# Performance work log

Hardware: AMD Instinct MI355X
Metric: run time of the kernel (lower is better)

The kernel has to match this reference:

```python
import jax, jax.numpy as jnp
import numpy as np

TOP_K = 50
MIN_KEEP = 5
TOP_P = 0.8
TEMPERATURE = 1.0
PENALTY = 1.1
LN_EPS = 1e-5

B, HIST, H, V = 32, 2048, 2048, 128000


def setup_inputs() -> dict:
    key = jax.random.key(0)
    k1, k2, k3, k4, k5 = jax.random.split(key, 5)
    hidden_states = jax.random.normal(k1, (B, H), dtype=jnp.float32)
    input_ids = jax.random.randint(k2, (B, HIST), 0, V, dtype=jnp.int64)
    ln_gamma = 1.0 + 0.02 * jax.random.normal(k3, (H,), dtype=jnp.float32)
    ln_beta = 0.02 * jax.random.normal(k4, (H,), dtype=jnp.float32)
    W = 0.02 * jax.random.normal(k5, (V, H), dtype=jnp.float32)  # lm_head weight [vocab, hidden]
    return {"input_ids": input_ids, "hidden_states": hidden_states,
            "ln_gamma": ln_gamma, "ln_beta": ln_beta, "W": W}


def reference(input_ids, hidden_states, ln_gamma, ln_beta, W):
    # ln_f: LayerNorm over hidden dim
    mu = jnp.mean(hidden_states, axis=-1, keepdims=True)
    var = jnp.mean(jnp.square(hidden_states - mu), axis=-1, keepdims=True)
    h = (hidden_states - mu) * jax.lax.rsqrt(var + LN_EPS) * ln_gamma + ln_beta
    # lm_head: [B,H] @ [H,V] -> [B,V]
    m_logits = jnp.einsum('bh,vh->bv', h, W)
    # repetition penalty: gather logits at history ids, penalize, scatter back
    g = jnp.take_along_axis(m_logits, input_ids, axis=1)          # [B, HIST]
    pen = jnp.where(g < 0, g * PENALTY, g / PENALTY)
    m_logits = jax.vmap(lambda row, idx, val: row.at[idx].set(val))(m_logits, input_ids, pen)
    # top-k, temperature, nucleus (top-p) masking
    vals, token = jax.lax.top_k(m_logits.astype(jnp.float32), TOP_K)  # [B, TOP_K]
    vals = vals / TEMPERATURE
    cum = jnp.cumsum(jax.nn.softmax(vals, axis=1), axis=1)
    keep = jnp.arange(TOP_K) < MIN_KEEP                            # keep_matrix row
    mask = (cum < TOP_P) | keep
    filtered = jnp.where(mask, vals, jnp.float32(-1000.0))
    probs = jax.nn.softmax(filtered, axis=1)
    return (probs, token)
```

## Files before the change

kernel.cpp:

```cpp
#include <hip/hip_runtime.h>
#include <math.h>

#define B_    32
#define H_    2048
#define V_    128000
#define HIST_ 2048
#define TOPK  50

__global__ __launch_bounds__(256) void ln_kernel(const float* __restrict__ x,
        const float* __restrict__ gamma, const float* __restrict__ beta,
        float* __restrict__ h) {
    int b = blockIdx.x, t = threadIdx.x;
    const float* xr = x + b * H_;
    __shared__ float red[4];
    __shared__ float sval;
    float s = 0.f;
    for (int k = t; k < H_; k += 256) s += xr[k];
    #pragma unroll
    for (int o = 32; o; o >>= 1) s += __shfl_down(s, o);
    if ((t & 63) == 0) red[t >> 6] = s;
    __syncthreads();
    if (t == 0) sval = (red[0] + red[1] + red[2] + red[3]) * (1.f / H_);
    __syncthreads();
    float mu = sval;
    float v = 0.f;
    for (int k = t; k < H_; k += 256) { float d = xr[k] - mu; v += d * d; }
    #pragma unroll
    for (int o = 32; o; o >>= 1) v += __shfl_down(v, o);
    if ((t & 63) == 0) red[t >> 6] = v;
    __syncthreads();
    if (t == 0) sval = 1.f / sqrtf((red[0] + red[1] + red[2] + red[3]) * (1.f / H_) + 1e-5f);
    __syncthreads();
    float rstd = sval;
    for (int k = t; k < H_; k += 256)
        h[b * H_ + k] = (xr[k] - mu) * rstd * gamma[k] + beta[k];
}

#define VT  256
#define KC  32
#define NCH (H_ / KC)

__global__ __launch_bounds__(256, 2) void gemm_kernel(const float* __restrict__ Wm,
        const float* __restrict__ hs, float* __restrict__ logits) {
    __shared__ float ldsW[VT * KC];
    __shared__ float ldsH[KC * B_];
    const int t  = threadIdx.x;
    const int v0 = blockIdx.x * VT;

    float acc[B_];
    #pragma unroll
    for (int i = 0; i < B_; i++) acc[i] = 0.f;

    float4 wreg[8];
    float4 hreg;
    const int hb = t >> 3, hk = (t & 7) * 4;

    #pragma unroll
    for (int i = 0; i < 8; i++) {
        int g = i * 256 + t, r = g >> 3, p = g & 7;
        wreg[i] = *(const float4*)(Wm + (size_t)(v0 + r) * H_ + p * 4);
    }
    hreg = *(const float4*)(hs + hb * H_ + hk);

    for (int c = 0; c < NCH; c++) {
        #pragma unroll
        for (int i = 0; i < 8; i++) {
            int g = i * 256 + t, r = g >> 3, p = g & 7;
            *(float4*)&ldsW[r * KC + ((p ^ (r & 7)) << 2)] = wreg[i];
        }
        ldsH[(hk + 0) * B_ + hb] = hreg.x;
        ldsH[(hk + 1) * B_ + hb] = hreg.y;
        ldsH[(hk + 2) * B_ + hb] = hreg.z;
        ldsH[(hk + 3) * B_ + hb] = hreg.w;
        __syncthreads();

        if (c + 1 < NCH) {
            int kn = (c + 1) * KC;
            #pragma unroll
            for (int i = 0; i < 8; i++) {
                int g = i * 256 + t, r = g >> 3, p = g & 7;
                wreg[i] = *(const float4*)(Wm + (size_t)(v0 + r) * H_ + kn + p * 4);
            }
            hreg = *(const float4*)(hs + hb * H_ + kn + hk);
        }

        for (int q = 0; q < KC / 4; q++) {
            float4 w4 = *(const float4*)&ldsW[t * KC + ((q ^ (t & 7)) << 2)];
            float wk[4] = {w4.x, w4.y, w4.z, w4.w};
            #pragma unroll
            for (int j = 0; j < 4; j++) {
                const float4* hp = (const float4*)&ldsH[(q * 4 + j) * B_];
                #pragma unroll
                for (int g2 = 0; g2 < 8; g2++) {
                    float4 hv = hp[g2];
                    acc[g2 * 4 + 0] += wk[j] * hv.x;
                    acc[g2 * 4 + 1] += wk[j] * hv.y;
                    acc[g2 * 4 + 2] += wk[j] * hv.z;
                    acc[g2 * 4 + 3] += wk[j] * hv.w;
                }
            }
        }
        __syncthreads();
    }

    const int v = v0 + t;
    #pragma unroll
    for (int b = 0; b < B_; b++)
        logits[(size_t)b * V_ + v] = acc[b];
}

__global__ __launch_bounds__(256) void pen_gather(const int* __restrict__ ids,
        const float* __restrict__ logits, float* __restrict__ pen) {
    int i = blockIdx.x * 256 + threadIdx.x;
    int b = i >> 11;
    int id = ids[i];
    float g = logits[(size_t)b * V_ + id];
    pen[i] = (g < 0.f) ? g * 1.1f : g / 1.1f;
}
__global__ __launch_bounds__(256) void pen_scatter(const int* __restrict__ ids,
        float* __restrict__ logits, const float* __restrict__ pen) {
    int i = blockIdx.x * 256 + threadIdx.x;
    int b = i >> 11;
    logits[(size_t)b * V_ + ids[i]] = pen[i];
}

__device__ __forceinline__ unsigned f2k(float f) {
    unsigned u = __float_as_uint(f);
    return (u >> 31) ? ~u : (u | 0x80000000u);
}
__device__ __forceinline__ float k2f(unsigned k) {
    return __uint_as_float((k >> 31) ? (k ^ 0x80000000u) : ~k);
}

__global__ __launch_bounds__(256) void topk_kernel(const float* __restrict__ logits,
        float* __restrict__ out) {
    int b = blockIdx.x, t = threadIdx.x;
    const float* row = logits + (size_t)b * V_;
    __shared__ int hist[256];
    __shared__ int sB1, sC1, sB2, sNa, sNe;
    __shared__ unsigned gtK[64];  __shared__ int gtI[64];
    __shared__ unsigned eqK[256]; __shared__ int eqI[256];
    __shared__ float outv[TOPK];  __shared__ int outi[TOPK];

    hist[t] = 0;
    __syncthreads();
    for (int v = t; v < V_; v += 256) atomicAdd(&hist[f2k(row[v]) >> 24], 1);
    __syncthreads();
    if (t == 0) {
        int c = 0, i = 255;
        for (; i >= 0; i--) { if (c + hist[i] >= TOPK) break; c += hist[i]; }
        sB1 = i; sC1 = c;
    }
    __syncthreads();
    unsigned b1 = (unsigned)sB1; int c1 = sC1;

    hist[t] = 0;
    __syncthreads();
    for (int v = t; v < V_; v += 256) {
        unsigned k = f2k(row[v]);
        if ((k >> 24) == b1) atomicAdd(&hist[(k >> 16) & 255], 1);
    }
    __syncthreads();
    if (t == 0) {
        int c = c1, i = 255;
        for (; i >= 0; i--) { if (c + hist[i] >= TOPK) break; c += hist[i]; }
        sB2 = i; sNa = 0; sNe = 0;
    }
    __syncthreads();
    unsigned pref = (b1 << 8) | (unsigned)sB2;

    for (int v = t; v < V_; v += 256) {
        unsigned k = f2k(row[v]);
        unsigned t16 = k >> 16;
        if (t16 > pref)       { int p = atomicAdd(&sNa, 1); if (p < 64)  { gtK[p] = k; gtI[p] = v; } }
        else if (t16 == pref) { int p = atomicAdd(&sNe, 1); if (p < 256) { eqK[p] = k; eqI[p] = v; } }
    }
    __syncthreads();

    if (t == 0) {
        int na = sNa; if (na > TOPK) na = TOPK;
        for (int i = 1; i < na; i++) {
            unsigned k = gtK[i]; int id = gtI[i]; int j = i - 1;
            for (; j >= 0 && (gtK[j] < k || (gtK[j] == k && gtI[j] > id)); j--) {
                gtK[j + 1] = gtK[j]; gtI[j + 1] = gtI[j];
            }
            gtK[j + 1] = k; gtI[j + 1] = id;
        }
        for (int i = 0; i < na; i++) { outv[i] = k2f(gtK[i]); outi[i] = gtI[i]; }
        int ne = sNe; if (ne > 256) ne = 256;
        for (int s = na; s < TOPK; s++) {
            int best = -1; unsigned bk = 0; int bi = 0x7fffffff;
            for (int i = 0; i < ne; i++) {
                if (eqI[i] < 0) continue;
                if (best < 0 || eqK[i] > bk || (eqK[i] == bk && eqI[i] < bi)) {
                    best = i; bk = eqK[i]; bi = eqI[i];
                }
            }
            outv[s] = k2f(bk); outi[s] = bi; eqI[best] = -1;
        }
    }
    __syncthreads();

    if (t < 64) {
        int i = t;
        float m  = outv[0];
        float vi = (i < TOPK) ? outv[i] : 0.f;
        float e  = (i < TOPK) ? expf(vi - m) : 0.f;
        float tot = e;
        #pragma unroll
        for (int o = 1; o < 64; o <<= 1) tot += __shfl_xor(tot, o);
        float p = e / tot;
        float pre = p;
        #pragma unroll
        for (int o = 1; o < 64; o <<= 1) { float u = __shfl_up(pre, o); if (t >= o) pre += u; }
        bool keep = (pre < 0.8f) || (i < 5);
        float f  = keep ? vi : -1000.f;
        float e2 = (i < TOPK) ? expf(f - m) : 0.f;
        float tot2 = e2;
        #pragma unroll
        for (int o = 1; o < 64; o <<= 1) tot2 += __shfl_xor(tot2, o);
        if (i < TOPK) {
            out[b * TOPK + i] = e2 / tot2;
            out[B_ * TOPK + b * TOPK + i] = (float)outi[i];
        }
    }
}

extern "C" void kernel_launch(void* const* d_in, const int* in_sizes, int n_in,
                              void* d_out, int out_size, void* d_ws, size_t ws_size,
                              hipStream_t stream) {
    const int*   ids    = (const int*)d_in[0];
    const float* hidden = (const float*)d_in[1];
    const float* gamma  = (const float*)d_in[2];
    const float* beta   = (const float*)d_in[3];
    const float* Wm     = (const float*)d_in[4];
    float* out = (float*)d_out;

    char* ws = (char*)d_ws;
    float* h      = (float*)ws;
    float* logits = (float*)(ws + 262144);
    float* pen    = (float*)(ws + 262144 + 16384000);

    ln_kernel  <<<B_,        256, 0, stream>>>(hidden, gamma, beta, h);
    gemm_kernel<<<V_ / VT,   256, 0, stream>>>(Wm, h, logits);
    pen_gather <<<(B_*HIST_)/256, 256, 0, stream>>>(ids, logits, pen);
    pen_scatter<<<(B_*HIST_)/256, 256, 0, stream>>>(ids, logits, pen);
    topk_kernel<<<B_,        256, 0, stream>>>(logits, out);
}
```

Baseline: 2.009 ms.

## Split top-k across row slices and retile GEMM inner loop per thread

```diff
diff --git a/kernel.cpp b/kernel.cpp
--- a/kernel.cpp
+++ b/kernel.cpp
@@ -6,11 +6,16 @@
 #define V_    128000
 #define HIST_ 2048
 #define TOPK  50
+#define CAP_EQ 8192
+#define NSLICE 16
+#define SLICE_ (V_ / NSLICE)
 
 __global__ __launch_bounds__(256) void ln_kernel(const float* __restrict__ x,
         const float* __restrict__ gamma, const float* __restrict__ beta,
-        float* __restrict__ h) {
+        float* __restrict__ h, int* __restrict__ ghist, int* __restrict__ meta) {
     int b = blockIdx.x, t = threadIdx.x;
+    ghist[b * 256 + t] = 0;
+    if (t < 8) meta[b * 8 + t] = 0;
     const float* xr = x + b * H_;
     __shared__ float red[4];
     __shared__ float sval;
@@ -46,10 +51,14 @@
     __shared__ float ldsH[KC * B_];
     const int t  = threadIdx.x;
     const int v0 = blockIdx.x * VT;
-
-    float acc[B_];
-    #pragma unroll
-    for (int i = 0; i < B_; i++) acc[i] = 0.f;
+    const int vt = t >> 2;
+    const int bg = (t & 3) * 8;
+
+    float acc[4][8];
+    #pragma unroll
+    for (int r = 0; r < 4; r++)
+        #pragma unroll
+        for (int j = 0; j < 8; j++) acc[r][j] = 0.f;
 
     float4 wreg[8];
     float4 hreg;
@@ -85,28 +94,34 @@
         }
 
         for (int q = 0; q < KC / 4; q++) {
-            float4 w4 = *(const float4*)&ldsW[t * KC + ((q ^ (t & 7)) << 2)];
-            float wk[4] = {w4.x, w4.y, w4.z, w4.w};
+            const int ws = ((q ^ (vt & 7)) << 2);
+            float4 w0 = *(const float4*)&ldsW[(vt      ) * KC + ws];
+            float4 w1 = *(const float4*)&ldsW[(vt +  64) * KC + ws];
+            float4 w2 = *(const float4*)&ldsW[(vt + 128) * KC + ws];
+            float4 w3 = *(const float4*)&ldsW[(vt + 192) * KC + ws];
             #pragma unroll
             for (int j = 0; j < 4; j++) {
-                const float4* hp = (const float4*)&ldsH[(q * 4 + j) * B_];
-                #pragma unroll
-                for (int g2 = 0; g2 < 8; g2++) {
-                    float4 hv = hp[g2];
-                    acc[g2 * 4 + 0] += wk[j] * hv.x;
-                    acc[g2 * 4 + 1] += wk[j] * hv.y;
-                    acc[g2 * 4 + 2] += wk[j] * hv.z;
-                    acc[g2 * 4 + 3] += wk[j] * hv.w;
-                }
+                float4 h0 = *(const float4*)&ldsH[(q * 4 + j) * B_ + bg];
+                float4 h1 = *(const float4*)&ldsH[(q * 4 + j) * B_ + bg + 4];
+                #define STEP(R, W4) { float wv = (&W4.x)[j];                  \
+                    acc[R][0] += wv * h0.x; acc[R][1] += wv * h0.y;           \
+                    acc[R][2] += wv * h0.z; acc[R][3] += wv * h0.w;           \
+                    acc[R][4] += wv * h1.x; acc[R][5] += wv * h1.y;           \
+                    acc[R][6] += wv * h1.z; acc[R][7] += wv * h1.w; }
+                STEP(0, w0) STEP(1, w1) STEP(2, w2) STEP(3, w3)
+                #undef STEP
             }
         }
         __syncthreads();
     }
 
-    const int v = v0 + t;
-    #pragma unroll
-    for (int b = 0; b < B_; b++)
-        logits[(size_t)b * V_ + v] = acc[b];
+    #pragma unroll
+    for (int r = 0; r < 4; r++) {
+        int v = v0 + vt + 64 * r;
+        #pragma unroll
+        for (int j = 0; j < 8; j++)
+            logits[(size_t)(bg + j) * V_ + v] = acc[r][j];
+    }
 }
 
 __global__ __launch_bounds__(256) void pen_gather(const int* __restrict__ ids,
@@ -132,71 +147,128 @@
     return __uint_as_float((k >> 31) ? (k ^ 0x80000000u) : ~k);
 }
 
-__global__ __launch_bounds__(256) void topk_kernel(const float* __restrict__ logits,
-        float* __restrict__ out) {
-    int b = blockIdx.x, t = threadIdx.x;
-    const float* row = logits + (size_t)b * V_;
+__global__ __launch_bounds__(256) void topk_hist(const float* __restrict__ logits,
+        int* __restrict__ ghist) {
+    int row = blockIdx.y, t = threadIdx.x;
     __shared__ int hist[256];
-    __shared__ int sB1, sC1, sB2, sNa, sNe;
-    __shared__ unsigned gtK[64];  __shared__ int gtI[64];
-    __shared__ unsigned eqK[256]; __shared__ int eqI[256];
-    __shared__ float outv[TOPK];  __shared__ int outi[TOPK];
-
     hist[t] = 0;
     __syncthreads();
-    for (int v = t; v < V_; v += 256) atomicAdd(&hist[f2k(row[v]) >> 24], 1);
+    const float4* rp = (const float4*)(logits + (size_t)row * V_);
+    int i0 = blockIdx.x * (SLICE_ / 4);
+    for (int i = i0 + t; i < i0 + SLICE_ / 4; i += 256) {
+        float4 v = rp[i];
+        atomicAdd(&hist[f2k(v.x) >> 24], 1);
+        atomicAdd(&hist[f2k(v.y) >> 24], 1);
+        atomicAdd(&hist[f2k(v.z) >> 24], 1);
+        atomicAdd(&hist[f2k(v.w) >> 24], 1);
+    }
+    __syncthreads();
+    if (hist[t]) atomicAdd(&ghist[row * 256 + t], hist[t]);
+}
+
+__global__ __launch_bounds__(256) void topk_collect(const float* __restrict__ logits,
+        const int* __restrict__ ghist, int* __restrict__ meta,
+        unsigned* __restrict__ sK, int* __restrict__ sI,
+        unsigned* __restrict__ eK, int* __restrict__ eI) {
+    int row = blockIdx.y, t = threadIdx.x;
+    __shared__ int lh[256];
+    __shared__ int sb1;
+    lh[t] = ghist[row * 256 + t];
     __syncthreads();
     if (t == 0) {
         int c = 0, i = 255;
+        for (; i >= 0; i--) { if (c + lh[i] >= TOPK) break; c += lh[i]; }
+        sb1 = i;
+    }
+    __syncthreads();
+    unsigned b1 = (unsigned)sb1;
+    const float4* rp = (const float4*)(logits + (size_t)row * V_);
+    int i0 = blockIdx.x * (SLICE_ / 4);
+    int* nA = &meta[row * 8 + 0];
+    int* nE = &meta[row * 8 + 1];
+    unsigned* ek = eK + (size_t)row * CAP_EQ;
+    int*      ei = eI + (size_t)row * CAP_EQ;
+    for (int i = i0 + t; i < i0 + SLICE_ / 4; i += 256) {
+        float4 v = rp[i];
+        float vv[4] = {v.x, v.y, v.z, v.w};
+        #pragma unroll
+        for (int u = 0; u < 4; u++) {
+            unsigned k = f2k(vv[u]);
+            unsigned by = k >> 24;
+            if (by >= b1) {
+                int idx = i * 4 + u;
+                if (by > b1) {
+                    int p = atomicAdd(nA, 1);
+                    if (p < 64) { sK[row * 64 + p] = k; sI[row * 64 + p] = idx; }
+                } else {
+                    int p = atomicAdd(nE, 1);
+                    if (p < CAP_EQ) { ek[p] = k; ei[p] = idx; }
+                }
+            }
+        }
+    }
+}
+
+__global__ __launch_bounds__(256) void topk_final(const int* __restrict__ meta,
+        const unsigned* __restrict__ sK, const int* __restrict__ sI,
+        const unsigned* __restrict__ eK, const int* __restrict__ eI,
+        float* __restrict__ out) {
+    int row = blockIdx.x, t = threadIdx.x;
+    __shared__ int hist[256];
+    __shared__ int sb2, scnt, sne2;
+    __shared__ unsigned gK[64]; __shared__ int gI[64];
+    __shared__ unsigned bK[256]; __shared__ int bI[256];
+    __shared__ float outv[TOPK]; __shared__ int outi[TOPK];
+
+    int nA = meta[row * 8 + 0]; if (nA > 64) nA = 64;
+    int nE = meta[row * 8 + 1]; if (nE > CAP_EQ) nE = CAP_EQ;
+
+    hist[t] = 0;
+    __syncthreads();
+    const unsigned* ek = eK + (size_t)row * CAP_EQ;
+    const int*      ei = eI + (size_t)row * CAP_EQ;
+    for (int i = t; i < nE; i += 256) atomicAdd(&hist[(ek[i] >> 16) & 255], 1);
+    __syncthreads();
+    if (t == 0) {
+        int c = nA, i = 255;
         for (; i >= 0; i--) { if (c + hist[i] >= TOPK) break; c += hist[i]; }
-        sB1 = i; sC1 = c;
-    }
-    __syncthreads();
-    unsigned b1 = (unsigned)sB1; int c1 = sC1;
-
-    hist[t] = 0;
-    __syncthreads();
-    for (int v = t; v < V_; v += 256) {
-        unsigned k = f2k(row[v]);
-        if ((k >> 24) == b1) atomicAdd(&hist[(k >> 16) & 255], 1);
-    }
-    __syncthreads();
+        sb2 = i; scnt = nA; sne2 = 0;
+    }
+    __syncthreads();
+    unsigned b2 = (unsigned)sb2;
+    if (t < nA) { gK[t] = sK[row * 64 + t]; gI[t] = sI[row * 64 + t]; }
+    for (int i = t; i < nE; i += 256) {
+        unsigned by = (ek[i] >> 16) & 255;
+        if (by > b2) {
+            int p = atomicAdd(&scnt, 1);
+            if (p < 64) { gK[p] = ek[i]; gI[p] = ei[i]; }
+        } else if (by == b2) {
+            int p = atomicAdd(&sne2, 1);
+            if (p < 256) { bK[p] = ek[i]; bI[p] = ei[i]; }
+        }
+    }
+    __syncthreads();
+
     if (t == 0) {
-        int c = c1, i = 255;
-        for (; i >= 0; i--) { if (c + hist[i] >= TOPK) break; c += hist[i]; }
-        sB2 = i; sNa = 0; sNe = 0;
-    }
-    __syncthreads();
-    unsigned pref = (b1 << 8) | (unsigned)sB2;
-
-    for (int v = t; v < V_; v += 256) {
-        unsigned k = f2k(row[v]);
-        unsigned t16 = k >> 16;
-        if (t16 > pref)       { int p = atomicAdd(&sNa, 1); if (p < 64)  { gtK[p] = k; gtI[p] = v; } }
-        else if (t16 == pref) { int p = atomicAdd(&sNe, 1); if (p < 256) { eqK[p] = k; eqI[p] = v; } }
-    }
-    __syncthreads();
-
-    if (t == 0) {
-        int na = sNa; if (na > TOPK) na = TOPK;
+        int na = scnt; if (na > TOPK) na = TOPK;
         for (int i = 1; i < na; i++) {
-            unsigned k = gtK[i]; int id = gtI[i]; int j = i - 1;
-            for (; j >= 0 && (gtK[j] < k || (gtK[j] == k && gtI[j] > id)); j--) {
-                gtK[j + 1] = gtK[j]; gtI[j + 1] = gtI[j];
-            }
-            gtK[j + 1] = k; gtI[j + 1] = id;
-        }
-        for (int i = 0; i < na; i++) { outv[i] = k2f(gtK[i]); outi[i] = gtI[i]; }
-        int ne = sNe; if (ne > 256) ne = 256;
+            unsigned k = gK[i]; int id = gI[i]; int j = i - 1;
+            for (; j >= 0 && (gK[j] < k || (gK[j] == k && gI[j] > id)); j--) {
+                gK[j + 1] = gK[j]; gI[j + 1] = gI[j];
+            }
+            gK[j + 1] = k; gI[j + 1] = id;
+        }
+        for (int i = 0; i < na; i++) { outv[i] = k2f(gK[i]); outi[i] = gI[i]; }
+        int ne = sne2; if (ne > 256) ne = 256;
         for (int s = na; s < TOPK; s++) {
             int best = -1; unsigned bk = 0; int bi = 0x7fffffff;
             for (int i = 0; i < ne; i++) {
-                if (eqI[i] < 0) continue;
-                if (best < 0 || eqK[i] > bk || (eqK[i] == bk && eqI[i] < bi)) {
-                    best = i; bk = eqK[i]; bi = eqI[i];
+                if (bI[i] < 0) continue;
+                if (best < 0 || bK[i] > bk || (bK[i] == bk && bI[i] < bi)) {
+                    best = i; bk = bK[i]; bi = bI[i];
                 }
             }
-            outv[s] = k2f(bk); outi[s] = bi; eqI[best] = -1;
+            outv[s] = k2f(bk); outi[s] = bi; bI[best] = -1;
         }
     }
     __syncthreads();
@@ -220,8 +292,8 @@
         #pragma unroll
         for (int o = 1; o < 64; o <<= 1) tot2 += __shfl_xor(tot2, o);
         if (i < TOPK) {
-            out[b * TOPK + i] = e2 / tot2;
-            out[B_ * TOPK + b * TOPK + i] = (float)outi[i];
+            out[row * TOPK + i] = e2 / tot2;
+            out[B_ * TOPK + row * TOPK + i] = (float)outi[i];
         }
     }
 }
@@ -237,13 +309,24 @@
     float* out = (float*)d_out;
 
     char* ws = (char*)d_ws;
-    float* h      = (float*)ws;
-    float* logits = (float*)(ws + 262144);
-    float* pen    = (float*)(ws + 262144 + 16384000);
-
-    ln_kernel  <<<B_,        256, 0, stream>>>(hidden, gamma, beta, h);
-    gemm_kernel<<<V_ / VT,   256, 0, stream>>>(Wm, h, logits);
-    pen_gather <<<(B_*HIST_)/256, 256, 0, stream>>>(ids, logits, pen);
-    pen_scatter<<<(B_*HIST_)/256, 256, 0, stream>>>(ids, logits, pen);
-    topk_kernel<<<B_,        256, 0, stream>>>(logits, out);
-}
+    size_t off = 0;
+    float* h      = (float*)(ws + off); off += 262144;
+    float* logits = (float*)(ws + off); off += 16384000;
+    float* pen    = (float*)(ws + off); off += 262144;
+    int*   ghist  = (int*)  (ws + off); off += 32768;
+    int*   meta   = (int*)  (ws + off); off += 1024;
+    unsigned* sK  = (unsigned*)(ws + off); off += B_ * 64 * 4;
+    int*   sI     = (int*)  (ws + off); off += B_ * 64 * 4;
+    unsigned* eK  = (unsigned*)(ws + off); off += (size_t)B_ * CAP_EQ * 4;
+    int*   eI     = (int*)  (ws + off); off += (size_t)B_ * CAP_EQ * 4;
+
+    dim3 gslice(NSLICE, B_);
+
+    ln_kernel   <<<B_,        256, 0, stream>>>(hidden, gamma, beta, h, ghist, meta);
+    gemm_kernel <<<V_ / VT,   256, 0, stream>>>(Wm, h, logits);
+    pen_gather  <<<(B_*HIST_)/256, 256, 0, stream>>>(ids, logits, pen);
+    pen_scatter <<<(B_*HIST_)/256, 256, 0, stream>>>(ids, logits, pen);
+    topk_hist   <<<gslice,    256, 0, stream>>>(logits, ghist);
+    topk_collect<<<gslice,    256, 0, stream>>>(logits, ghist, meta, sK, sI, eK, eI);
+    topk_final  <<<B_,        256, 0, stream>>>(meta, sK, sI, eK, eI, out);
+}
```

New measurement: 1.733 ms. 13.7% less time.
